# Kernel tuning notes

Measured on AMD Instinct MI355X. Metric: run time of the kernel, lower is better.

## Reference

```python
import jax, jax.numpy as jnp
import numpy as np

TEMPERATURE = 8.0  # sqrt(d_k=64)

def setup_inputs() -> dict:
    key = jax.random.key(0)
    kq, kk, kv = jax.random.split(key, 3)
    B, S, D = 32, 8192, 64
    q = jax.random.normal(kq, (B, D), dtype=jnp.float32)
    k = jax.random.normal(kk, (B, S, D), dtype=jnp.float32)
    v = jax.random.normal(kv, (B, S, D), dtype=jnp.float32)
    return {"q": q, "k": k, "v": v}

def reference(q, k, v):
    # attn scores: [B, 1, S] = q[B,1,D] @ k^T[B,D,S]
    attn = jnp.einsum('bd,bsd->bs', q, k) / TEMPERATURE  # [B, S]
    attn = jax.nn.softmax(attn, axis=-1)
    # dropout is identity in eval / deterministic reference
    out = jnp.einsum('bs,bsd->bd', attn, v)  # [B, D]
    # match torch shapes: output [B,1,D], attn [B,1,S]
    return out[:, None, :], attn[:, None, :]
```

## Files before the change

### kernel.cpp

```cpp
#include <hip/hip_runtime.h>

#define NB 32
#define NS 8192
#define ND 64
#define CHUNK 256
#define NCHUNK (NS / CHUNK)
#define INV_T 0.125f
#define PSTRIDE 66

__global__ __launch_bounds__(256) void attn_p1(
    const float* __restrict__ q, const float* __restrict__ k,
    const float* __restrict__ v, float* __restrict__ attn,
    float* __restrict__ part)
{
    const int blk = blockIdx.x;
    const int b   = blk >> 5;
    const int c   = blk & (NCHUNK - 1);
    const int tid = threadIdx.x;
    const int w   = tid >> 6;
    const int l   = tid & 63;
    const int l16 = l & 15;
    const int g   = l >> 4;

    const float4 qv = *reinterpret_cast<const float4*>(q + b * ND + l16 * 4);

    const size_t kb = (size_t)b * NS * ND;
    const int rows_base = c * CHUNK + w * 64 + g * 16;

    float s[16];
#pragma unroll
    for (int i = 0; i < 16; ++i) {
        const float4 kv = *reinterpret_cast<const float4*>(
            k + kb + (size_t)(rows_base + i) * ND + l16 * 4);
        float p = qv.x * kv.x + qv.y * kv.y + qv.z * kv.z + qv.w * kv.w;
        p += __shfl_xor(p, 1);
        p += __shfl_xor(p, 2);
        p += __shfl_xor(p, 4);
        p += __shfl_xor(p, 8);
        s[i] = p * INV_T;
    }

    attn[(size_t)b * NS + c * CHUNK + tid] = s[l16];

    float m = s[0];
#pragma unroll
    for (int i = 1; i < 16; ++i) m = fmaxf(m, s[i]);

    __shared__ float redm[16];
    __shared__ float redl[16];
    __shared__ float accl[4][ND];

    if (l16 == 0) redm[w * 4 + g] = m;
    __syncthreads();
    float mc = redm[0];
#pragma unroll
    for (int i = 1; i < 16; ++i) mc = fmaxf(mc, redm[i]);

    float lsum = 0.f;
    float4 acc = make_float4(0.f, 0.f, 0.f, 0.f);
#pragma unroll
    for (int i = 0; i < 16; ++i) {
        const float e = __expf(s[i] - mc);
        lsum += e;
        const float4 vv = *reinterpret_cast<const float4*>(
            v + kb + (size_t)(rows_base + i) * ND + l16 * 4);
        acc.x += e * vv.x; acc.y += e * vv.y;
        acc.z += e * vv.z; acc.w += e * vv.w;
    }

    if (l16 == 0) redl[w * 4 + g] = lsum;

    acc.x += __shfl_xor(acc.x, 16); acc.y += __shfl_xor(acc.y, 16);
    acc.z += __shfl_xor(acc.z, 16); acc.w += __shfl_xor(acc.w, 16);
    acc.x += __shfl_xor(acc.x, 32); acc.y += __shfl_xor(acc.y, 32);
    acc.z += __shfl_xor(acc.z, 32); acc.w += __shfl_xor(acc.w, 32);
    if (l < 16) {
        accl[w][l16 * 4 + 0] = acc.x;
        accl[w][l16 * 4 + 1] = acc.y;
        accl[w][l16 * 4 + 2] = acc.z;
        accl[w][l16 * 4 + 3] = acc.w;
    }
    __syncthreads();

    float* pp = part + (size_t)blk * PSTRIDE;
    if (tid == 0) {
        float lt = 0.f;
        for (int i = 0; i < 16; ++i) lt += redl[i];
        pp[0] = mc;
        pp[1] = lt;
    }
    if (tid < ND) {
        pp[2 + tid] = accl[0][tid] + accl[1][tid] + accl[2][tid] + accl[3][tid];
    }
}

__global__ __launch_bounds__(64) void attn_p2(
    const float* __restrict__ part, float* __restrict__ out,
    float* __restrict__ stats)
{
    const int b = blockIdx.x;
    const int t = threadIdx.x;
    const float* pb = part + (size_t)b * NCHUNK * PSTRIDE;

    float m = -1e30f;
    for (int c = 0; c < NCHUNK; ++c) m = fmaxf(m, pb[c * PSTRIDE]);

    float lsum = 0.f, acc = 0.f;
    for (int c = 0; c < NCHUNK; ++c) {
        const float wgt = __expf(pb[c * PSTRIDE] - m);
        lsum += pb[c * PSTRIDE + 1] * wgt;
        acc  += pb[c * PSTRIDE + 2 + t] * wgt;
    }
    const float invl = 1.f / lsum;
    out[b * ND + t] = acc * invl;
    if (t == 0) { stats[b * 2] = m; stats[b * 2 + 1] = invl; }
}

__global__ __launch_bounds__(256) void attn_p3(
    float* __restrict__ attn, const float* __restrict__ stats)
{
    const int idx = blockIdx.x * 256 + threadIdx.x;
    const int b = idx >> 11;
    const float m    = stats[b * 2];
    const float invl = stats[b * 2 + 1];
    float4 sv = reinterpret_cast<float4*>(attn)[idx];
    sv.x = __expf(sv.x - m) * invl;
    sv.y = __expf(sv.y - m) * invl;
    sv.z = __expf(sv.z - m) * invl;
    sv.w = __expf(sv.w - m) * invl;
    reinterpret_cast<float4*>(attn)[idx] = sv;
}

extern "C" void kernel_launch(void* const* d_in, const int* in_sizes, int n_in,
                              void* d_out, int out_size, void* d_ws, size_t ws_size,
                              hipStream_t stream)
{
    const float* q = (const float*)d_in[0];
    const float* k = (const float*)d_in[1];
    const float* v = (const float*)d_in[2];

    float* out  = (float*)d_out;
    float* attn = out + NB * ND;

    float* part  = (float*)d_ws;
    float* stats = part + (size_t)NB * NCHUNK * PSTRIDE;

    attn_p1<<<NB * NCHUNK, 256, 0, stream>>>(q, k, v, attn, part);
    attn_p2<<<NB, 64, 0, stream>>>(part, out, stats);
    attn_p3<<<(NB * NS / 4) / 256, 256, 0, stream>>>(attn, stats);
}
```

Measured before the change: 33.69 us.

## Compute QK scores one row per thread with q staged in LDS

The QK dot product is restructured so each thread computes a full 64-wide dot product for one key row from a q vector staged in shared memory. This replaces the 16-lane shuffle reductions, and the row max and sum now use wave-wide shuffles. The exp weights go into an LDS array that the PV loop reads. This removes many cross-lane shuffles, but the K loads become strided per thread (256B apart), which can hurt coalescing, and it adds an extra barrier.

```diff
diff --git a/kernel.cpp b/kernel.cpp
--- a/kernel.cpp
+++ b/kernel.cpp
@@ -22,53 +22,58 @@
     const int l16 = l & 15;
     const int g   = l >> 4;
 
-    const float4 qv = *reinterpret_cast<const float4*>(q + b * ND + l16 * 4);
-
-    const size_t kb = (size_t)b * NS * ND;
-    const int rows_base = c * CHUNK + w * 64 + g * 16;
-
-    float s[16];
-#pragma unroll
-    for (int i = 0; i < 16; ++i) {
-        const float4 kv = *reinterpret_cast<const float4*>(
-            k + kb + (size_t)(rows_base + i) * ND + l16 * 4);
-        float p = qv.x * kv.x + qv.y * kv.y + qv.z * kv.z + qv.w * kv.w;
-        p += __shfl_xor(p, 1);
-        p += __shfl_xor(p, 2);
-        p += __shfl_xor(p, 4);
-        p += __shfl_xor(p, 8);
-        s[i] = p * INV_T;
-    }
-
-    attn[(size_t)b * NS + c * CHUNK + tid] = s[l16];
-
-    float m = s[0];
-#pragma unroll
-    for (int i = 1; i < 16; ++i) m = fmaxf(m, s[i]);
-
-    __shared__ float redm[16];
-    __shared__ float redl[16];
+    __shared__ float qlds[ND];
+    __shared__ float es[CHUNK];
+    __shared__ float redm[4];
+    __shared__ float redl[4];
     __shared__ float accl[4][ND];
 
-    if (l16 == 0) redm[w * 4 + g] = m;
+    if (tid < ND / 4) {
+        reinterpret_cast<float4*>(qlds)[tid] =
+            reinterpret_cast<const float4*>(q + b * ND)[tid];
+    }
     __syncthreads();
-    float mc = redm[0];
+
+    const size_t kb  = (size_t)b * NS * ND;
+    const int    row = c * CHUNK + tid;
+    const float4* krow = reinterpret_cast<const float4*>(k + kb + (size_t)row * ND);
+
+    float4 a = make_float4(0.f, 0.f, 0.f, 0.f);
 #pragma unroll
-    for (int i = 1; i < 16; ++i) mc = fmaxf(mc, redm[i]);
+    for (int j = 0; j < 16; ++j) {
+        const float4 kv = krow[j];
+        const float4 qv = reinterpret_cast<float4*>(qlds)[j];
+        a.x += kv.x * qv.x; a.y += kv.y * qv.y;
+        a.z += kv.z * qv.z; a.w += kv.w * qv.w;
+    }
+    const float s = (a.x + a.y + a.z + a.w) * INV_T;
+    attn[(size_t)b * NS + row] = s;
 
-    float lsum = 0.f;
+    float m = s;
+#pragma unroll
+    for (int d = 1; d < 64; d <<= 1) m = fmaxf(m, __shfl_xor(m, d));
+    if (l == 0) redm[w] = m;
+    __syncthreads();
+    const float mc = fmaxf(fmaxf(redm[0], redm[1]), fmaxf(redm[2], redm[3]));
+
+    const float e = __expf(s - mc);
+    es[tid] = e;
+    float ls = e;
+#pragma unroll
+    for (int d = 1; d < 64; d <<= 1) ls += __shfl_xor(ls, d);
+    if (l == 0) redl[w] = ls;
+    __syncthreads();
+
+    const int rbase = w * 64 + g * 16;
     float4 acc = make_float4(0.f, 0.f, 0.f, 0.f);
 #pragma unroll
     for (int i = 0; i < 16; ++i) {
-        const float e = __expf(s[i] - mc);
-        lsum += e;
-        const float4 vv = *reinterpret_cast<const float4*>(
-            v + kb + (size_t)(rows_base + i) * ND + l16 * 4);
-        acc.x += e * vv.x; acc.y += e * vv.y;
-        acc.z += e * vv.z; acc.w += e * vv.w;
+        const float ei = es[rbase + i];
+        const float4 vv = reinterpret_cast<const float4*>(
+            v + kb + (size_t)(c * CHUNK + rbase + i) * ND)[l16];
+        acc.x += ei * vv.x; acc.y += ei * vv.y;
+        acc.z += ei * vv.z; acc.w += ei * vv.w;
     }
-
-    if (l16 == 0) redl[w * 4 + g] = lsum;
 
     acc.x += __shfl_xor(acc.x, 16); acc.y += __shfl_xor(acc.y, 16);
     acc.z += __shfl_xor(acc.z, 16); acc.w += __shfl_xor(acc.w, 16);
@@ -84,10 +89,8 @@
 
     float* pp = part + (size_t)blk * PSTRIDE;
     if (tid == 0) {
-        float lt = 0.f;
-        for (int i = 0; i < 16; ++i) lt += redl[i];
         pp[0] = mc;
-        pp[1] = lt;
+        pp[1] = redl[0] + redl[1] + redl[2] + redl[3];
     }
     if (tid < ND) {
         pp[2 + tid] = accl[0][tid] + accl[1][tid] + accl[2][tid] + accl[3][tid];
```

Result: slower. 36.44 us (+8.1%).

## Prefetch K and V into registers, drop block syncs, emit per-wave partials

Applied to the files above, without the earlier changes.

Phase 1 now issues all K and V loads for a thread's 16 rows up front, so the V load latency overlaps the dot products. The two __syncthreads and the shared-memory reductions are replaced by wave-level shuffle reductions, and each wave writes its own partial (max, sum, accumulator) into a padded stride-68 slot. Phase 2 grows to 256 threads and merges four times as many partials with a cross-wave shared reduction. The cost is much higher register use in phase 1, which could lower occupancy, plus more partial data for phase 2 to read.

```diff
diff --git a/kernel.cpp b/kernel.cpp
--- a/kernel.cpp
+++ b/kernel.cpp
@@ -6,7 +6,8 @@
 #define CHUNK 256
 #define NCHUNK (NS / CHUNK)
 #define INV_T 0.125f
-#define PSTRIDE 66
+#define PSTRIDE 68
+#define NPART_PER_B (NCHUNK * 4)
 
 __global__ __launch_bounds__(256) void attn_p1(
     const float* __restrict__ q, const float* __restrict__ k,
@@ -22,98 +23,106 @@
     const int l16 = l & 15;
     const int g   = l >> 4;
 
-    const float4 qv = *reinterpret_cast<const float4*>(q + b * ND + l16 * 4);
+    const size_t kb    = (size_t)b * NS * ND;
+    const int    rbase = c * CHUNK + w * 64 + g * 16;
 
-    const size_t kb = (size_t)b * NS * ND;
-    const int rows_base = c * CHUNK + w * 64 + g * 16;
+    const float4  qv = *reinterpret_cast<const float4*>(q + b * ND + l16 * 4);
+    const float4* kp = reinterpret_cast<const float4*>(k + kb);
+    const float4* vp = reinterpret_cast<const float4*>(v + kb);
+
+    float4 kf[16], vf[16];
+#pragma unroll
+    for (int j = 0; j < 16; ++j)
+        kf[j] = kp[(size_t)(rbase + j) * (ND / 4) + l16];
+#pragma unroll
+    for (int j = 0; j < 16; ++j)
+        vf[j] = vp[(size_t)(rbase + j) * (ND / 4) + l16];
+    asm volatile("" ::: "memory");
 
     float s[16];
 #pragma unroll
-    for (int i = 0; i < 16; ++i) {
-        const float4 kv = *reinterpret_cast<const float4*>(
-            k + kb + (size_t)(rows_base + i) * ND + l16 * 4);
-        float p = qv.x * kv.x + qv.y * kv.y + qv.z * kv.z + qv.w * kv.w;
+    for (int j = 0; j < 16; ++j) {
+        float p = kf[j].x * qv.x + kf[j].y * qv.y +
+                  kf[j].z * qv.z + kf[j].w * qv.w;
         p += __shfl_xor(p, 1);
         p += __shfl_xor(p, 2);
         p += __shfl_xor(p, 4);
         p += __shfl_xor(p, 8);
-        s[i] = p * INV_T;
+        s[j] = p * INV_T;
     }
 
-    attn[(size_t)b * NS + c * CHUNK + tid] = s[l16];
+    float sc = s[0];
+#pragma unroll
+    for (int j = 1; j < 16; ++j) sc = (l16 == j) ? s[j] : sc;
+    attn[(size_t)b * NS + c * CHUNK + w * 64 + l] = sc;
 
     float m = s[0];
 #pragma unroll
-    for (int i = 1; i < 16; ++i) m = fmaxf(m, s[i]);
+    for (int j = 1; j < 16; ++j) m = fmaxf(m, s[j]);
+    m = fmaxf(m, __shfl_xor(m, 16));
+    m = fmaxf(m, __shfl_xor(m, 32));
 
-    __shared__ float redm[16];
-    __shared__ float redl[16];
-    __shared__ float accl[4][ND];
+    float e[16];
+    float ls = 0.f;
+#pragma unroll
+    for (int j = 0; j < 16; ++j) { e[j] = __expf(s[j] - m); ls += e[j]; }
+    ls += __shfl_xor(ls, 16);
+    ls += __shfl_xor(ls, 32);
 
-    if (l16 == 0) redm[w * 4 + g] = m;
-    __syncthreads();
-    float mc = redm[0];
-#pragma unroll
-    for (int i = 1; i < 16; ++i) mc = fmaxf(mc, redm[i]);
-
-    float lsum = 0.f;
     float4 acc = make_float4(0.f, 0.f, 0.f, 0.f);
 #pragma unroll
-    for (int i = 0; i < 16; ++i) {
-        const float e = __expf(s[i] - mc);
-        lsum += e;
-        const float4 vv = *reinterpret_cast<const float4*>(
-            v + kb + (size_t)(rows_base + i) * ND + l16 * 4);
-        acc.x += e * vv.x; acc.y += e * vv.y;
-        acc.z += e * vv.z; acc.w += e * vv.w;
+    for (int j = 0; j < 16; ++j) {
+        acc.x += e[j] * vf[j].x; acc.y += e[j] * vf[j].y;
+        acc.z += e[j] * vf[j].z; acc.w += e[j] * vf[j].w;
     }
-
-    if (l16 == 0) redl[w * 4 + g] = lsum;
-
     acc.x += __shfl_xor(acc.x, 16); acc.y += __shfl_xor(acc.y, 16);
     acc.z += __shfl_xor(acc.z, 16); acc.w += __shfl_xor(acc.w, 16);
     acc.x += __shfl_xor(acc.x, 32); acc.y += __shfl_xor(acc.y, 32);
     acc.z += __shfl_xor(acc.z, 32); acc.w += __shfl_xor(acc.w, 32);
-    if (l < 16) {
-        accl[w][l16 * 4 + 0] = acc.x;
-        accl[w][l16 * 4 + 1] = acc.y;
-        accl[w][l16 * 4 + 2] = acc.z;
-        accl[w][l16 * 4 + 3] = acc.w;
-    }
-    __syncthreads();
 
-    float* pp = part + (size_t)blk * PSTRIDE;
-    if (tid == 0) {
-        float lt = 0.f;
-        for (int i = 0; i < 16; ++i) lt += redl[i];
-        pp[0] = mc;
-        pp[1] = lt;
-    }
-    if (tid < ND) {
-        pp[2 + tid] = accl[0][tid] + accl[1][tid] + accl[2][tid] + accl[3][tid];
-    }
+    float* pp = part + (size_t)(blk * 4 + w) * PSTRIDE;
+    if (l == 0) { pp[0] = m; pp[1] = ls; }
+    if (l < 16) reinterpret_cast<float4*>(pp + 4)[l16] = acc;
 }
 
-__global__ __launch_bounds__(64) void attn_p2(
+__global__ __launch_bounds__(256) void attn_p2(
     const float* __restrict__ part, float* __restrict__ out,
     float* __restrict__ stats)
 {
     const int b = blockIdx.x;
-    const int t = threadIdx.x;
-    const float* pb = part + (size_t)b * NCHUNK * PSTRIDE;
+    const int w = threadIdx.x >> 6;
+    const int l = threadIdx.x & 63;
+    const float* pb = part + (size_t)b * NPART_PER_B * PSTRIDE;
+
+    __shared__ float wm[4], wl[4], wacc[4][ND];
 
     float m = -1e30f;
-    for (int c = 0; c < NCHUNK; ++c) m = fmaxf(m, pb[c * PSTRIDE]);
+#pragma unroll 8
+    for (int i = 0; i < 32; ++i)
+        m = fmaxf(m, pb[(w * 32 + i) * PSTRIDE]);
+    if (l == 0) wm[w] = m;
+    __syncthreads();
+    const float M = fmaxf(fmaxf(wm[0], wm[1]), fmaxf(wm[2], wm[3]));
 
-    float lsum = 0.f, acc = 0.f;
-    for (int c = 0; c < NCHUNK; ++c) {
-        const float wgt = __expf(pb[c * PSTRIDE] - m);
-        lsum += pb[c * PSTRIDE + 1] * wgt;
-        acc  += pb[c * PSTRIDE + 2 + t] * wgt;
+    float ls = 0.f, acc = 0.f;
+#pragma unroll 8
+    for (int i = 0; i < 32; ++i) {
+        const float* pe = pb + (w * 32 + i) * PSTRIDE;
+        const float wgt = __expf(pe[0] - M);
+        ls  += pe[1] * wgt;
+        acc += pe[4 + l] * wgt;
     }
-    const float invl = 1.f / lsum;
-    out[b * ND + t] = acc * invl;
-    if (t == 0) { stats[b * 2] = m; stats[b * 2 + 1] = invl; }
+    if (l == 0) wl[w] = ls;
+    wacc[w][l] = acc;
+    __syncthreads();
+
+    if (w == 0) {
+        const float lt = wl[0] + wl[1] + wl[2] + wl[3];
+        const float a  = wacc[0][l] + wacc[1][l] + wacc[2][l] + wacc[3][l];
+        const float invl = 1.f / lt;
+        out[b * ND + l] = a * invl;
+        if (l == 0) { stats[b * 2] = M; stats[b * 2 + 1] = invl; }
+    }
 }
 
 __global__ __launch_bounds__(256) void attn_p3(
@@ -143,9 +152,9 @@
     float* attn = out + NB * ND;
 
     float* part  = (float*)d_ws;
-    float* stats = part + (size_t)NB * NCHUNK * PSTRIDE;
+    float* stats = part + (size_t)NB * NCHUNK * 4 * PSTRIDE;
 
     attn_p1<<<NB * NCHUNK, 256, 0, stream>>>(q, k, v, attn, part);
-    attn_p2<<<NB, 64, 0, stream>>>(part, out, stats);
+    attn_p2<<<NB, 256, 0, stream>>>(part, out, stats);
     attn_p3<<<(NB * NS / 4) / 256, 256, 0, stream>>>(attn, stats);
 }
```

Result: slower. 39.11 us (+16.1%).
